# Optimization experiments

Measured on AMD Instinct MI355X. Metric: run time of the kernel, lower is better.

## Reference

```python
import jax, jax.numpy as jnp
import numpy as np

DROPOUT_RATE = 0.25
MASK_KEY = jax.random.key(42)

def _masks(key, shape, rate):
    keep = 1.0 - rate
    k1, k2, k3 = jax.random.split(key, 3)
    m = lambda k: jax.random.bernoulli(k, keep, shape).astype(jnp.float32) / keep
    return m(k1), m(k2), m(k3)  # out_mask, h_mask, c_mask

def _lstm_layer(x, W_ih, W_hh, b_ih, b_hh, layer_key, rate):
    # x: [B, T, D]; W_ih: [4H, D]; W_hh: [4H, H]
    B, T, _ = x.shape
    H = W_hh.shape[1]
    m_out, m_h, m_c = _masks(layer_key, (B, H), rate)  # variational: shared across time
    # Precompute input-to-gate projection for the whole sequence (one big GEMM).
    xg = jnp.einsum('btd,gd->tbg', x, W_ih) + (b_ih + b_hh)  # [T, B, 4H]

    def step(carry, xg_t):
        h, c = carry
        g = xg_t + h @ W_hh.T  # [B, 4H]
        i, f, gg, o = jnp.split(g, 4, axis=-1)
        i, f, o = jax.nn.sigmoid(i), jax.nn.sigmoid(f), jax.nn.sigmoid(o)
        c = f * c + i * jnp.tanh(gg)
        h = o * jnp.tanh(c)
        out = h * m_out
        return (h * m_h, c * m_c), out

    h0 = jnp.zeros((B, H), x.dtype)
    c0 = jnp.zeros((B, H), x.dtype)
    _, ys = jax.lax.scan(step, (h0, c0), xg)  # ys: [T, B, H]
    return jnp.transpose(ys, (1, 0, 2))  # [B, T, H]

def setup_inputs() -> dict:
    key = jax.random.key(0)
    ks = jax.random.split(key, 9)
    B, T, D, H = 64, 512, 256, 256
    s_ih = 1.0 / np.sqrt(D)
    s_hh = 1.0 / np.sqrt(H)
    return {
        'x': jax.random.normal(ks[0], (B, T, D), jnp.float32),
        'W_ih0': jax.random.uniform(ks[1], (4 * H, D), jnp.float32, -s_ih, s_ih),
        'W_hh0': jax.random.uniform(ks[2], (4 * H, H), jnp.float32, -s_hh, s_hh),
        'b_ih0': jax.random.uniform(ks[3], (4 * H,), jnp.float32, -s_hh, s_hh),
        'b_hh0': jax.random.uniform(ks[4], (4 * H,), jnp.float32, -s_hh, s_hh),
        'W_ih1': jax.random.uniform(ks[5], (4 * H, H), jnp.float32, -s_hh, s_hh),
        'W_hh1': jax.random.uniform(ks[6], (4 * H, H), jnp.float32, -s_hh, s_hh),
        'b_ih1': jax.random.uniform(ks[7], (4 * H,), jnp.float32, -s_hh, s_hh),
        'b_hh1': jax.random.uniform(ks[8], (4 * H,), jnp.float32, -s_hh, s_hh),
    }

def reference(x, W_ih0, W_hh0, b_ih0, b_hh0, W_ih1, W_hh1, b_ih1, b_hh1):
    k0, k1 = jax.random.split(MASK_KEY, 2)
    x = _lstm_layer(x, W_ih0, W_hh0, b_ih0, b_hh0, k0, DROPOUT_RATE)
    x = _lstm_layer(x, W_ih1, W_hh1, b_ih1, b_hh1, k1, DROPOUT_RATE)
    return x
```

## Files before the change

### kernel.cpp

```cpp
#include <hip/hip_runtime.h>

typedef unsigned int u32;
typedef unsigned short u16;

typedef short short8 __attribute__((ext_vector_type(8)));
typedef float f32x4 __attribute__((ext_vector_type(4)));


__device__ __forceinline__ float fast_exp2(float x) {
#if __has_builtin(__builtin_amdgcn_exp2f)
  return __builtin_amdgcn_exp2f(x);
#else
  return exp2f(x);
#endif
}
__device__ __forceinline__ float fast_rcp(float x) {
#if __has_builtin(__builtin_amdgcn_rcpf)
  return __builtin_amdgcn_rcpf(x);
#else
  return 1.0f / x;
#endif
}
__device__ __forceinline__ float sigmf_(float x) {
  return fast_rcp(1.0f + fast_exp2(-1.44269504088896f * x));
}
__device__ __forceinline__ float tanhf_(float x) {
  float e = fast_exp2(2.88539008177793f * x);
  return 1.0f - 2.0f * fast_rcp(e + 1.0f);
}
__device__ __forceinline__ u16 f2bf(float x) {
  u32 u = __float_as_uint(x);
  u32 r = (u + 0x7fffu + ((u >> 16) & 1u)) >> 16;
  return (u16)r;
}

#if __has_builtin(__builtin_amdgcn_fdot2_f32_bf16)
typedef __bf16 bf16x2_t __attribute__((ext_vector_type(2)));
__device__ __forceinline__ float dot2bf(u32 w, u32 h, float acc) {
  return __builtin_amdgcn_fdot2_f32_bf16(__builtin_bit_cast(bf16x2_t, w),
                                         __builtin_bit_cast(bf16x2_t, h), acc, false);
}
#else
__device__ __forceinline__ float dot2bf(u32 w, u32 h, float acc) {
  float wl = __uint_as_float(w << 16);
  float wh = __uint_as_float(w & 0xffff0000u);
  float hl = __uint_as_float(h << 16);
  float hh = __uint_as_float(h & 0xffff0000u);
  return fmaf(wh, hh, fmaf(wl, hl, acc));
}
#endif


__device__ __forceinline__ void tf_round(u32& x0, u32& x1, int r) {
  x0 += x1;
  x1 = (x1 << r) | (x1 >> (32 - r));
  x1 ^= x0;
}
__device__ void threefry(u32 k0, u32 k1, u32 c0, u32 c1, u32& o0, u32& o1) {
  u32 k2 = k0 ^ k1 ^ 0x1BD11BDAu;
  u32 x0 = c0 + k0, x1 = c1 + k1;
  tf_round(x0, x1, 13); tf_round(x0, x1, 15); tf_round(x0, x1, 26); tf_round(x0, x1, 6);
  x0 += k1; x1 += k2 + 1u;
  tf_round(x0, x1, 17); tf_round(x0, x1, 29); tf_round(x0, x1, 16); tf_round(x0, x1, 24);
  x0 += k2; x1 += k0 + 2u;
  tf_round(x0, x1, 13); tf_round(x0, x1, 15); tf_round(x0, x1, 26); tf_round(x0, x1, 6);
  x0 += k0; x1 += k1 + 3u;
  tf_round(x0, x1, 17); tf_round(x0, x1, 29); tf_round(x0, x1, 16); tf_round(x0, x1, 24);
  x0 += k1; x1 += k2 + 4u;
  tf_round(x0, x1, 13); tf_round(x0, x1, 15); tf_round(x0, x1, 26); tf_round(x0, x1, 6);
  x0 += k2; x1 += k0 + 5u;
  o0 = x0; o1 = x1;
}

#define JAX_PARTITIONABLE 1

__global__ void masks_kernel(float* __restrict__ masks) {
  int gid = blockIdx.x * 256 + threadIdx.x;
  if (gid >= 2 * 3 * 16384) return;
  int l = gid / 49152;
  int rem = gid - l * 49152;
  int typ = rem / 16384;
  int i = rem - typ * 16384;
  u32 bits;
#if JAX_PARTITIONABLE
  u32 lk0, lk1, mk0, mk1, y0, y1;
  threefry(0u, 42u, 0u, (u32)l, lk0, lk1);
  threefry(lk0, lk1, 0u, (u32)typ, mk0, mk1);
  threefry(mk0, mk1, 0u, (u32)i, y0, y1);
  bits = y0 ^ y1;
#else
  u32 a0, a1, b0, b1;
  threefry(0u, 42u, 0u, 2u, a0, a1);
  threefry(0u, 42u, 1u, 3u, b0, b1);
  u32 lk0 = (l == 0) ? a0 : a1;
  u32 lk1 = (l == 0) ? b0 : b1;
  u32 e00, e01, e10, e11, e20, e21;
  threefry(lk0, lk1, 0u, 3u, e00, e01);
  threefry(lk0, lk1, 1u, 4u, e10, e11);
  threefry(lk0, lk1, 2u, 5u, e20, e21);
  u32 mk0 = (typ == 0) ? e00 : (typ == 1) ? e20 : e11;
  u32 mk1 = (typ == 0) ? e10 : (typ == 1) ? e01 : e21;
  u32 p = (i < 8192) ? (u32)i : (u32)(i - 8192);
  u32 y0, y1;
  threefry(mk0, mk1, p, p + 8192u, y0, y1);
  bits = (i < 8192) ? y0 : y1;
#endif
  float u = __uint_as_float((bits >> 9) | 0x3f800000u) - 1.0f;
  masks[gid] = (u < 0.75f) ? (1.0f / 0.75f) : 0.0f;
}


__global__ void conv_bf16(const float* __restrict__ src, u16* __restrict__ dst, int n) {
  int gid = blockIdx.x * 256 + threadIdx.x;
  if (gid < n) dst[gid] = f2bf(src[gid]);
}

__global__ void pack_whh(const float* __restrict__ W, u32* __restrict__ Wp, u32* __restrict__ Ws) {
  int gid = blockIdx.x * 256 + threadIdx.x;
  int p = gid >> 10;
  int row = gid & 1023;
  u32 lo = f2bf(W[row * 256 + 2 * p]);
  u32 hi = f2bf(W[row * 256 + 2 * p + 1]);
  u32 v = lo | (hi << 16);
  Wp[p * 1024 + row] = v;
  if (p >= 112) Ws[row * 16 + (p - 112)] = v;
}

__global__ void add_bias(const float* __restrict__ a, const float* __restrict__ b,
                         float* __restrict__ o, int n) {
  int gid = blockIdx.x * 256 + threadIdx.x;
  if (gid < n) o[gid] = a[gid] + b[gid];
}

__global__ __launch_bounds__(256) void gemm_xg(const u16* __restrict__ A,
                                               const u16* __restrict__ Bw,
                                               float* __restrict__ xg) {
  __shared__ uint4 Als[2048];
  __shared__ uint4 Bls[2048];
  int tid = threadIdx.x;
  int m0 = blockIdx.x * 64;
  int n0 = blockIdx.y * 64;
  {
    int row = tid >> 2, kseg = tid & 3;
    const uint4* Ag = (const uint4*)(A + (size_t)(m0 + row) * 256);
    const uint4* Bg = (const uint4*)(Bw + (size_t)(n0 + row) * 256);
#pragma unroll
    for (int uu = 0; uu < 8; ++uu) {
      int kb = kseg * 8 + uu;
      Als[kb * 64 + row] = Ag[kb];
      Bls[kb * 64 + row] = Bg[kb];
    }
  }
  __syncthreads();
  int w = tid >> 6, l = tid & 63;
  int wm = (w >> 1) * 32, wn = (w & 1) * 32;
  int lm = l & 15, q = l >> 4;
  f32x4 acc00 = {0.f, 0.f, 0.f, 0.f}, acc01 = acc00, acc10 = acc00, acc11 = acc00;
#pragma unroll
  for (int ks = 0; ks < 8; ++ks) {
    int kb = ks * 4 + q;
    short8 a0 = __builtin_bit_cast(short8, Als[kb * 64 + wm + lm]);
    short8 a1 = __builtin_bit_cast(short8, Als[kb * 64 + wm + 16 + lm]);
    short8 b0 = __builtin_bit_cast(short8, Bls[kb * 64 + wn + lm]);
    short8 b1 = __builtin_bit_cast(short8, Bls[kb * 64 + wn + 16 + lm]);
    acc00 = __builtin_amdgcn_mfma_f32_16x16x32_bf16(a0, b0, acc00, 0, 0, 0);
    acc01 = __builtin_amdgcn_mfma_f32_16x16x32_bf16(a0, b1, acc01, 0, 0, 0);
    acc10 = __builtin_amdgcn_mfma_f32_16x16x32_bf16(a1, b0, acc10, 0, 0, 0);
    acc11 = __builtin_amdgcn_mfma_f32_16x16x32_bf16(a1, b1, acc11, 0, 0, 0);
  }
#pragma unroll
  for (int fm = 0; fm < 2; ++fm)
#pragma unroll
    for (int fn = 0; fn < 2; ++fn) {
      f32x4 acc = (fm == 0) ? ((fn == 0) ? acc00 : acc01) : ((fn == 0) ? acc10 : acc11);
#pragma unroll
      for (int r = 0; r < 4; ++r) {
        int m = m0 + wm + fm * 16 + q * 4 + r;
        int n = n0 + wn + fn * 16 + lm;
        int bb = m >> 9, tt = m & 511;
        xg[(size_t)tt * 65536 + (size_t)bb * 1024 + n] = acc[r];
      }
    }
}

#define REG_P 98
#define LDS_P 14

__global__ __launch_bounds__(512) void lstm_rec(
    const u32* __restrict__ Wp,
    const uint4* __restrict__ Ws,
    const float* __restrict__ xg,
    const float* __restrict__ bias,
    const float* __restrict__ masks,
    float* __restrict__ outF,
    u16* __restrict__ outB)
{
  __shared__ u32 Wl[LDS_P * 1024];
  __shared__ float gates[1024];
  __shared__ alignas(16) u16 hbf[256];

  const int tid = threadIdx.x;
  const int b = blockIdx.x;
  const int r0 = tid, r1 = tid + 512;

  u32 wreg[2 * REG_P];
#pragma unroll
  for (int p = 0; p < REG_P; ++p) wreg[p] = Wp[p * 1024 + r0];
#pragma unroll
  for (int p = 0; p < REG_P; ++p) wreg[REG_P + p] = Wp[p * 1024 + r1];

#pragma unroll
  for (int s = 0; s < LDS_P; ++s) {
    Wl[s * 1024 + r0] = Wp[(REG_P + s) * 1024 + r0];
    Wl[s * 1024 + r1] = Wp[(REG_P + s) * 1024 + r1];
  }
  if (tid < 256) hbf[tid] = 0;

  const float bias0 = bias[r0];
  const float bias1 = bias[r1];
  float c = 0.f, m_out = 0.f, m_h = 0.f, m_c = 0.f;
  if (tid < 256) {
    m_out = masks[0 * 16384 + b * 256 + tid];
    m_h   = masks[1 * 16384 + b * 256 + tid];
    m_c   = masks[2 * 16384 + b * 256 + tid];
  }
  const uint4* Wsr0 = Ws + (size_t)r0 * 4;
  const uint4* Wsr1 = Ws + (size_t)r1 * 4;
  const float* xgb = xg + b * 1024;
  float* outFb = outF ? outF + (size_t)b * 512 * 256 : (float*)0;
  u16* outBb = outB ? outB + (size_t)b * 512 * 256 : (u16*)0;

  __syncthreads();

  for (int t = 0; t < 512; ++t) {
    float xg0 = xgb[(size_t)t * 65536 + r0];
    float xg1 = xgb[(size_t)t * 65536 + r1];
    float acc0 = bias0, acc1 = bias1;
    const uint4* h4 = (const uint4*)hbf;
#pragma unroll
    for (int s4 = 0; s4 < 4; ++s4) {
      uint4 v0 = Wsr0[s4];
      uint4 v1 = Wsr1[s4];
      uint4 hp = h4[28 + s4];
      acc0 = dot2bf(v0.x, hp.x, acc0); acc1 = dot2bf(v1.x, hp.x, acc1);
      acc0 = dot2bf(v0.y, hp.y, acc0); acc1 = dot2bf(v1.y, hp.y, acc1);
      acc0 = dot2bf(v0.z, hp.z, acc0); acc1 = dot2bf(v1.z, hp.z, acc1);
      acc0 = dot2bf(v0.w, hp.w, acc0); acc1 = dot2bf(v1.w, hp.w, acc1);
    }
#pragma unroll
    for (int qq = 0; qq < 28; ++qq) {
      uint4 hp = h4[qq];
      u32 hh[4] = {hp.x, hp.y, hp.z, hp.w};
#pragma unroll
      for (int e = 0; e < 4; ++e) {
        const int p = qq * 4 + e;
        u32 w0, w1;
        if (p < REG_P) {
          w0 = wreg[p];
          w1 = wreg[REG_P + p];
        } else {
          w0 = Wl[(p - REG_P) * 1024 + r0];
          w1 = Wl[(p - REG_P) * 1024 + r1];
        }
        acc0 = dot2bf(w0, hh[e], acc0);
        acc1 = dot2bf(w1, hh[e], acc1);
      }
    }
    acc0 += xg0;
    acc1 += xg1;
    gates[r0] = acc0;
    gates[r1] = acc1;
    __syncthreads();
    if (tid < 256) {
      float gi = gates[tid];
      float gf = gates[tid + 256];
      float gg = gates[tid + 512];
      float go = gates[tid + 768];
      float fi = sigmf_(gi), ff = sigmf_(gf), fo = sigmf_(go);
      float tg = tanhf_(gg);
      c = ff * c + fi * tg;
      float hn = fo * tanhf_(c);
      float ov = hn * m_out;
      if (outFb) outFb[t * 256 + tid] = ov;
      if (outBb) outBb[t * 256 + tid] = f2bf(ov);
      hbf[tid] = f2bf(hn * m_h);
      c *= m_c;
    }
    __syncthreads();
  }
}


extern "C" void kernel_launch(void* const* d_in, const int* in_sizes, int n_in,
                              void* d_out, int out_size, void* d_ws, size_t ws_size,
                              hipStream_t stream) {
  const float* x    = (const float*)d_in[0];
  const float* Wih0 = (const float*)d_in[1];
  const float* Whh0 = (const float*)d_in[2];
  const float* bih0 = (const float*)d_in[3];
  const float* bhh0 = (const float*)d_in[4];
  const float* Wih1 = (const float*)d_in[5];
  const float* Whh1 = (const float*)d_in[6];
  const float* bih1 = (const float*)d_in[7];
  const float* bhh1 = (const float*)d_in[8];
  float* out = (float*)d_out;

  char* w = (char*)d_ws;
  float* masks = (float*)(w + 0);
  float* biasb = (float*)(w + 393216);
  u32* Wp0     = (u32*)(w + 401408);
  u32* Wp1     = (u32*)(w + 925696);
  u32* Ws0     = (u32*)(w + 1449984);
  u32* Ws1     = (u32*)(w + 1515520);
  u16* Wih0b   = (u16*)(w + 1581056);
  u16* Wih1b   = (u16*)(w + 2105344);
  u16* xb      = (u16*)(w + 2629632);
  u16* o1b     = (u16*)(w + 19406848);
  float* xg    = (float*)(w + 36184064);

  hipLaunchKernelGGL(masks_kernel, dim3(384), dim3(256), 0, stream, masks);
  hipLaunchKernelGGL(conv_bf16, dim3(32768), dim3(256), 0, stream, x, xb, 8388608);
  hipLaunchKernelGGL(conv_bf16, dim3(1024), dim3(256), 0, stream, Wih0, Wih0b, 262144);
  hipLaunchKernelGGL(conv_bf16, dim3(1024), dim3(256), 0, stream, Wih1, Wih1b, 262144);
  hipLaunchKernelGGL(pack_whh, dim3(512), dim3(256), 0, stream, Whh0, Wp0, Ws0);
  hipLaunchKernelGGL(pack_whh, dim3(512), dim3(256), 0, stream, Whh1, Wp1, Ws1);
  hipLaunchKernelGGL(add_bias, dim3(4), dim3(256), 0, stream, bih0, bhh0, biasb, 1024);
  hipLaunchKernelGGL(add_bias, dim3(4), dim3(256), 0, stream, bih1, bhh1, biasb + 1024, 1024);

  hipLaunchKernelGGL(gemm_xg, dim3(512, 16), dim3(256), 0, stream, xb, Wih0b, xg);
  hipLaunchKernelGGL(lstm_rec, dim3(64), dim3(512), 0, stream, Wp0, (const uint4*)Ws0, xg,
                     biasb, masks, (float*)nullptr, o1b);
  hipLaunchKernelGGL(gemm_xg, dim3(512, 16), dim3(256), 0, stream, o1b, Wih1b, xg);
  hipLaunchKernelGGL(lstm_rec, dim3(64), dim3(512), 0, stream, Wp1, (const uint4*)Ws1, xg,
                     biasb + 1024, masks + 49152, out, (u16*)nullptr);
}
```

Before: 1.944 ms.

## Give each recurrent thread all four gates of one unit to drop gate LDS sync

The recurrent kernel now runs 256 threads per batch row instead of 512. Each thread computes the i, f, g and o gate rows for one hidden unit and holds 96 packed weight pairs per gate in registers (384 VGPRs). The remaining 32 pairs per gate are streamed from a uint4-transposed global layout with double-buffered prefetch. Since the gate nonlinearity happens in the same thread, the shared gates array and one barrier per timestep go away, and h is double-buffered in LDS. This halves the thread count and greatly raises register pressure (risk of spills) to cut per-step synchronisation and idle half-block work.

```diff
diff --git a/kernel.cpp b/kernel.cpp
--- a/kernel.cpp
+++ b/kernel.cpp
@@ -115,15 +115,19 @@
   if (gid < n) dst[gid] = f2bf(src[gid]);
 }
 
-__global__ void pack_whh(const float* __restrict__ W, u32* __restrict__ Wp, u32* __restrict__ Ws) {
+__global__ void pack_whh(const float* __restrict__ W, u32* __restrict__ Wp, u32* __restrict__ Wst) {
   int gid = blockIdx.x * 256 + threadIdx.x;
   int p = gid >> 10;
   int row = gid & 1023;
   u32 lo = f2bf(W[row * 256 + 2 * p]);
   u32 hi = f2bf(W[row * 256 + 2 * p + 1]);
   u32 v = lo | (hi << 16);
-  Wp[p * 1024 + row] = v;
-  if (p >= 112) Ws[row * 16 + (p - 112)] = v;
+  if (p < 96) {
+    Wp[p * 1024 + row] = v;
+  } else {
+    int q = (p - 96) >> 2, e = (p - 96) & 3;
+    Wst[(q * 1024 + row) * 4 + e] = v;
+  }
 }
 
 __global__ void add_bias(const float* __restrict__ a, const float* __restrict__ b,
@@ -183,49 +187,41 @@
     }
 }
 
-#define REG_P 98
-#define LDS_P 14
-
-__global__ __launch_bounds__(512) void lstm_rec(
+#define REG_P 96
+
+__global__ __launch_bounds__(256, 1) void lstm_rec(
     const u32* __restrict__ Wp,
-    const uint4* __restrict__ Ws,
+    const uint4* __restrict__ Wst,
     const float* __restrict__ xg,
     const float* __restrict__ bias,
     const float* __restrict__ masks,
     float* __restrict__ outF,
     u16* __restrict__ outB)
 {
-  __shared__ u32 Wl[LDS_P * 1024];
-  __shared__ float gates[1024];
-  __shared__ alignas(16) u16 hbf[256];
+  __shared__ alignas(16) u16 hbf[2][256];
 
   const int tid = threadIdx.x;
   const int b = blockIdx.x;
-  const int r0 = tid, r1 = tid + 512;
-
-  u32 wreg[2 * REG_P];
-#pragma unroll
-  for (int p = 0; p < REG_P; ++p) wreg[p] = Wp[p * 1024 + r0];
-#pragma unroll
-  for (int p = 0; p < REG_P; ++p) wreg[REG_P + p] = Wp[p * 1024 + r1];
-
-#pragma unroll
-  for (int s = 0; s < LDS_P; ++s) {
-    Wl[s * 1024 + r0] = Wp[(REG_P + s) * 1024 + r0];
-    Wl[s * 1024 + r1] = Wp[(REG_P + s) * 1024 + r1];
-  }
-  if (tid < 256) hbf[tid] = 0;
-
-  const float bias0 = bias[r0];
-  const float bias1 = bias[r1];
-  float c = 0.f, m_out = 0.f, m_h = 0.f, m_c = 0.f;
-  if (tid < 256) {
-    m_out = masks[0 * 16384 + b * 256 + tid];
-    m_h   = masks[1 * 16384 + b * 256 + tid];
-    m_c   = masks[2 * 16384 + b * 256 + tid];
-  }
-  const uint4* Wsr0 = Ws + (size_t)r0 * 4;
-  const uint4* Wsr1 = Ws + (size_t)r1 * 4;
+
+  u32 wreg[4][REG_P];
+#pragma unroll
+  for (int g = 0; g < 4; ++g) {
+    const int row = tid + 256 * g;
+#pragma unroll
+    for (int p = 0; p < REG_P; ++p) wreg[g][p] = Wp[p * 1024 + row];
+  }
+
+  hbf[0][tid] = 0;
+
+  float biasv[4];
+#pragma unroll
+  for (int g = 0; g < 4; ++g) biasv[g] = bias[tid + 256 * g];
+
+  const float m_out = masks[0 * 16384 + b * 256 + tid];
+  const float m_h   = masks[1 * 16384 + b * 256 + tid];
+  const float m_c   = masks[2 * 16384 + b * 256 + tid];
+  float c = 0.f;
+
   const float* xgb = xg + b * 1024;
   float* outFb = outF ? outF + (size_t)b * 512 * 256 : (float*)0;
   u16* outBb = outB ? outB + (size_t)b * 512 * 256 : (u16*)0;
@@ -233,59 +229,63 @@
   __syncthreads();
 
   for (int t = 0; t < 512; ++t) {
-    float xg0 = xgb[(size_t)t * 65536 + r0];
-    float xg1 = xgb[(size_t)t * 65536 + r1];
-    float acc0 = bias0, acc1 = bias1;
-    const uint4* h4 = (const uint4*)hbf;
-#pragma unroll
-    for (int s4 = 0; s4 < 4; ++s4) {
-      uint4 v0 = Wsr0[s4];
-      uint4 v1 = Wsr1[s4];
-      uint4 hp = h4[28 + s4];
-      acc0 = dot2bf(v0.x, hp.x, acc0); acc1 = dot2bf(v1.x, hp.x, acc1);
-      acc0 = dot2bf(v0.y, hp.y, acc0); acc1 = dot2bf(v1.y, hp.y, acc1);
-      acc0 = dot2bf(v0.z, hp.z, acc0); acc1 = dot2bf(v1.z, hp.z, acc1);
-      acc0 = dot2bf(v0.w, hp.w, acc0); acc1 = dot2bf(v1.w, hp.w, acc1);
-    }
-#pragma unroll
-    for (int qq = 0; qq < 28; ++qq) {
-      uint4 hp = h4[qq];
-      u32 hh[4] = {hp.x, hp.y, hp.z, hp.w};
-#pragma unroll
-      for (int e = 0; e < 4; ++e) {
-        const int p = qq * 4 + e;
-        u32 w0, w1;
-        if (p < REG_P) {
-          w0 = wreg[p];
-          w1 = wreg[REG_P + p];
-        } else {
-          w0 = Wl[(p - REG_P) * 1024 + r0];
-          w1 = Wl[(p - REG_P) * 1024 + r1];
-        }
-        acc0 = dot2bf(w0, hh[e], acc0);
-        acc1 = dot2bf(w1, hh[e], acc1);
+    float xgv[4];
+#pragma unroll
+    for (int g = 0; g < 4; ++g) xgv[g] = xgb[(size_t)t * 65536 + tid + 256 * g];
+
+    const uint4* h4 = (const uint4*)hbf[t & 1];
+
+    float acc[4];
+#pragma unroll
+    for (int g = 0; g < 4; ++g) acc[g] = biasv[g];
+
+    uint4 tva[4], tvb[4];
+#pragma unroll
+    for (int g = 0; g < 4; ++g) tva[g] = Wst[0 * 1024 + tid + 256 * g];
+
+#pragma unroll
+    for (int q = 0; q < 24; ++q) {
+      uint4 hp = h4[q];
+#pragma unroll
+      for (int g = 0; g < 4; ++g) {
+        acc[g] = dot2bf(wreg[g][4 * q + 0], hp.x, acc[g]);
+        acc[g] = dot2bf(wreg[g][4 * q + 1], hp.y, acc[g]);
+        acc[g] = dot2bf(wreg[g][4 * q + 2], hp.z, acc[g]);
+        acc[g] = dot2bf(wreg[g][4 * q + 3], hp.w, acc[g]);
       }
     }
-    acc0 += xg0;
-    acc1 += xg1;
-    gates[r0] = acc0;
-    gates[r1] = acc1;
-    __syncthreads();
-    if (tid < 256) {
-      float gi = gates[tid];
-      float gf = gates[tid + 256];
-      float gg = gates[tid + 512];
-      float go = gates[tid + 768];
-      float fi = sigmf_(gi), ff = sigmf_(gf), fo = sigmf_(go);
-      float tg = tanhf_(gg);
-      c = ff * c + fi * tg;
-      float hn = fo * tanhf_(c);
-      float ov = hn * m_out;
-      if (outFb) outFb[t * 256 + tid] = ov;
-      if (outBb) outBb[t * 256 + tid] = f2bf(ov);
-      hbf[tid] = f2bf(hn * m_h);
-      c *= m_c;
+
+#pragma unroll
+    for (int q = 0; q < 8; ++q) {
+      uint4* curv = (q & 1) ? tvb : tva;
+      uint4* nxtv = (q & 1) ? tva : tvb;
+      if (q < 7) {
+#pragma unroll
+        for (int g = 0; g < 4; ++g) nxtv[g] = Wst[(q + 1) * 1024 + tid + 256 * g];
+      }
+      uint4 hp = h4[24 + q];
+#pragma unroll
+      for (int g = 0; g < 4; ++g) {
+        acc[g] = dot2bf(curv[g].x, hp.x, acc[g]);
+        acc[g] = dot2bf(curv[g].y, hp.y, acc[g]);
+        acc[g] = dot2bf(curv[g].z, hp.z, acc[g]);
+        acc[g] = dot2bf(curv[g].w, hp.w, acc[g]);
+      }
     }
+
+    float gi = acc[0] + xgv[0];
+    float gf = acc[1] + xgv[1];
+    float gg = acc[2] + xgv[2];
+    float go = acc[3] + xgv[3];
+    float fi = sigmf_(gi), ff = sigmf_(gf), fo = sigmf_(go);
+    float tg = tanhf_(gg);
+    c = ff * c + fi * tg;
+    float hn = fo * tanhf_(c);
+    float ov = hn * m_out;
+    if (outFb) outFb[t * 256 + tid] = ov;
+    if (outBb) outBb[t * 256 + tid] = f2bf(ov);
+    hbf[(t + 1) & 1][tid] = f2bf(hn * m_h);
+    c *= m_c;
     __syncthreads();
   }
 }
@@ -309,28 +309,28 @@
   float* masks = (float*)(w + 0);
   float* biasb = (float*)(w + 393216);
   u32* Wp0     = (u32*)(w + 401408);
-  u32* Wp1     = (u32*)(w + 925696);
-  u32* Ws0     = (u32*)(w + 1449984);
-  u32* Ws1     = (u32*)(w + 1515520);
-  u16* Wih0b   = (u16*)(w + 1581056);
-  u16* Wih1b   = (u16*)(w + 2105344);
-  u16* xb      = (u16*)(w + 2629632);
-  u16* o1b     = (u16*)(w + 19406848);
-  float* xg    = (float*)(w + 36184064);
+  u32* Wp1     = (u32*)(w + 794624);
+  u32* Wst0    = (u32*)(w + 1187840);
+  u32* Wst1    = (u32*)(w + 1318912);
+  u16* Wih0b   = (u16*)(w + 1449984);
+  u16* Wih1b   = (u16*)(w + 1974272);
+  u16* xb      = (u16*)(w + 2498560);
+  u16* o1b     = (u16*)(w + 19275776);
+  float* xg    = (float*)(w + 36052992);
 
   hipLaunchKernelGGL(masks_kernel, dim3(384), dim3(256), 0, stream, masks);
   hipLaunchKernelGGL(conv_bf16, dim3(32768), dim3(256), 0, stream, x, xb, 8388608);
   hipLaunchKernelGGL(conv_bf16, dim3(1024), dim3(256), 0, stream, Wih0, Wih0b, 262144);
   hipLaunchKernelGGL(conv_bf16, dim3(1024), dim3(256), 0, stream, Wih1, Wih1b, 262144);
-  hipLaunchKernelGGL(pack_whh, dim3(512), dim3(256), 0, stream, Whh0, Wp0, Ws0);
-  hipLaunchKernelGGL(pack_whh, dim3(512), dim3(256), 0, stream, Whh1, Wp1, Ws1);
+  hipLaunchKernelGGL(pack_whh, dim3(512), dim3(256), 0, stream, Whh0, Wp0, Wst0);
+  hipLaunchKernelGGL(pack_whh, dim3(512), dim3(256), 0, stream, Whh1, Wp1, Wst1);
   hipLaunchKernelGGL(add_bias, dim3(4), dim3(256), 0, stream, bih0, bhh0, biasb, 1024);
   hipLaunchKernelGGL(add_bias, dim3(4), dim3(256), 0, stream, bih1, bhh1, biasb + 1024, 1024);
 
   hipLaunchKernelGGL(gemm_xg, dim3(512, 16), dim3(256), 0, stream, xb, Wih0b, xg);
-  hipLaunchKernelGGL(lstm_rec, dim3(64), dim3(512), 0, stream, Wp0, (const uint4*)Ws0, xg,
+  hipLaunchKernelGGL(lstm_rec, dim3(64), dim3(256), 0, stream, Wp0, (const uint4*)Wst0, xg,
                      biasb, masks, (float*)nullptr, o1b);
   hipLaunchKernelGGL(gemm_xg, dim3(512, 16), dim3(256), 0, stream, o1b, Wih1b, xg);
-  hipLaunchKernelGGL(lstm_rec, dim3(64), dim3(512), 0, stream, Wp1, (const uint4*)Ws1, xg,
+  hipLaunchKernelGGL(lstm_rec, dim3(64), dim3(256), 0, stream, Wp1, (const uint4*)Wst1, xg,
                      biasb + 1024, masks + 49152, out, (u16*)nullptr);
 }
```

Result: slower. 5.716 ms (+194.0%).

## Use 1024-thread recurrent blocks with one gate row per thread in registers

Applied to the files above, without the earlier changes.

The recurrent kernel now launches 1024 threads per batch element, so each thread owns one gate row. Its 128 packed bf16 weight pairs are held entirely in registers as 32 uint4, which removes the LDS weight tier and the separate global 'Ws' tail read on every step. The W_hh packing is changed to a q-major uint4 layout to match, and the next step's xg value is prefetched one iteration ahead. In exchange, each block now has twice as many waves syncing at every step, and only 256 of the 1024 threads do the elementwise gate work.

```diff
diff --git a/kernel.cpp b/kernel.cpp
--- a/kernel.cpp
+++ b/kernel.cpp
@@ -115,15 +115,15 @@
   if (gid < n) dst[gid] = f2bf(src[gid]);
 }
 
-__global__ void pack_whh(const float* __restrict__ W, u32* __restrict__ Wp, u32* __restrict__ Ws) {
+__global__ void pack_whh(const float* __restrict__ W, u32* __restrict__ Wq) {
   int gid = blockIdx.x * 256 + threadIdx.x;
   int p = gid >> 10;
   int row = gid & 1023;
   u32 lo = f2bf(W[row * 256 + 2 * p]);
   u32 hi = f2bf(W[row * 256 + 2 * p + 1]);
   u32 v = lo | (hi << 16);
-  Wp[p * 1024 + row] = v;
-  if (p >= 112) Ws[row * 16 + (p - 112)] = v;
+  int q = p >> 2, e = p & 3;
+  Wq[(q * 1024 + row) * 4 + e] = v;
 }
 
 __global__ void add_bias(const float* __restrict__ a, const float* __restrict__ b,
@@ -183,94 +183,59 @@
     }
 }
 
-#define REG_P 98
-#define LDS_P 14
-
-__global__ __launch_bounds__(512) void lstm_rec(
-    const u32* __restrict__ Wp,
-    const uint4* __restrict__ Ws,
+__global__ __launch_bounds__(1024, 4) void lstm_rec(
+    const uint4* __restrict__ Wq,
     const float* __restrict__ xg,
     const float* __restrict__ bias,
     const float* __restrict__ masks,
     float* __restrict__ outF,
     u16* __restrict__ outB)
 {
-  __shared__ u32 Wl[LDS_P * 1024];
   __shared__ float gates[1024];
   __shared__ alignas(16) u16 hbf[256];
 
   const int tid = threadIdx.x;
   const int b = blockIdx.x;
-  const int r0 = tid, r1 = tid + 512;
-
-  u32 wreg[2 * REG_P];
-#pragma unroll
-  for (int p = 0; p < REG_P; ++p) wreg[p] = Wp[p * 1024 + r0];
-#pragma unroll
-  for (int p = 0; p < REG_P; ++p) wreg[REG_P + p] = Wp[p * 1024 + r1];
-
-#pragma unroll
-  for (int s = 0; s < LDS_P; ++s) {
-    Wl[s * 1024 + r0] = Wp[(REG_P + s) * 1024 + r0];
-    Wl[s * 1024 + r1] = Wp[(REG_P + s) * 1024 + r1];
-  }
+
+  uint4 w[32];
+#pragma unroll
+  for (int q = 0; q < 32; ++q) w[q] = Wq[q * 1024 + tid];
+
   if (tid < 256) hbf[tid] = 0;
 
-  const float bias0 = bias[r0];
-  const float bias1 = bias[r1];
+  const float biasv = bias[tid];
   float c = 0.f, m_out = 0.f, m_h = 0.f, m_c = 0.f;
   if (tid < 256) {
     m_out = masks[0 * 16384 + b * 256 + tid];
     m_h   = masks[1 * 16384 + b * 256 + tid];
     m_c   = masks[2 * 16384 + b * 256 + tid];
   }
-  const uint4* Wsr0 = Ws + (size_t)r0 * 4;
-  const uint4* Wsr1 = Ws + (size_t)r1 * 4;
-  const float* xgb = xg + b * 1024;
-  float* outFb = outF ? outF + (size_t)b * 512 * 256 : (float*)0;
-  u16* outBb = outB ? outB + (size_t)b * 512 * 256 : (u16*)0;
-
+
+  const float* xgp = xg + b * 1024 + tid;
+  float* outFp = outF ? outF + (size_t)b * 512 * 256 + tid : (float*)0;
+  u16* outBp = outB ? outB + (size_t)b * 512 * 256 + tid : (u16*)0;
+
+  float xg_next = xgp[0];
   __syncthreads();
 
+#pragma unroll 1
   for (int t = 0; t < 512; ++t) {
-    float xg0 = xgb[(size_t)t * 65536 + r0];
-    float xg1 = xgb[(size_t)t * 65536 + r1];
-    float acc0 = bias0, acc1 = bias1;
+    float xgv = xg_next;
+    if (t < 511) xg_next = xgp[(size_t)(t + 1) * 65536];
+
     const uint4* h4 = (const uint4*)hbf;
-#pragma unroll
-    for (int s4 = 0; s4 < 4; ++s4) {
-      uint4 v0 = Wsr0[s4];
-      uint4 v1 = Wsr1[s4];
-      uint4 hp = h4[28 + s4];
-      acc0 = dot2bf(v0.x, hp.x, acc0); acc1 = dot2bf(v1.x, hp.x, acc1);
-      acc0 = dot2bf(v0.y, hp.y, acc0); acc1 = dot2bf(v1.y, hp.y, acc1);
-      acc0 = dot2bf(v0.z, hp.z, acc0); acc1 = dot2bf(v1.z, hp.z, acc1);
-      acc0 = dot2bf(v0.w, hp.w, acc0); acc1 = dot2bf(v1.w, hp.w, acc1);
-    }
-#pragma unroll
-    for (int qq = 0; qq < 28; ++qq) {
-      uint4 hp = h4[qq];
-      u32 hh[4] = {hp.x, hp.y, hp.z, hp.w};
-#pragma unroll
-      for (int e = 0; e < 4; ++e) {
-        const int p = qq * 4 + e;
-        u32 w0, w1;
-        if (p < REG_P) {
-          w0 = wreg[p];
-          w1 = wreg[REG_P + p];
-        } else {
-          w0 = Wl[(p - REG_P) * 1024 + r0];
-          w1 = Wl[(p - REG_P) * 1024 + r1];
-        }
-        acc0 = dot2bf(w0, hh[e], acc0);
-        acc1 = dot2bf(w1, hh[e], acc1);
-      }
-    }
-    acc0 += xg0;
-    acc1 += xg1;
-    gates[r0] = acc0;
-    gates[r1] = acc1;
+    float acc = biasv;
+#pragma unroll
+    for (int q = 0; q < 32; ++q) {
+      uint4 hp = h4[q];
+      acc = dot2bf(w[q].x, hp.x, acc);
+      acc = dot2bf(w[q].y, hp.y, acc);
+      acc = dot2bf(w[q].z, hp.z, acc);
+      acc = dot2bf(w[q].w, hp.w, acc);
+    }
+    gates[tid] = acc + xgv;
     __syncthreads();
+
     if (tid < 256) {
       float gi = gates[tid];
       float gf = gates[tid + 256];
@@ -281,8 +246,8 @@
       c = ff * c + fi * tg;
       float hn = fo * tanhf_(c);
       float ov = hn * m_out;
-      if (outFb) outFb[t * 256 + tid] = ov;
-      if (outBb) outBb[t * 256 + tid] = f2bf(ov);
+      if (outFp) outFp[t * 256] = ov;
+      if (outBp) outBp[t * 256] = f2bf(ov);
       hbf[tid] = f2bf(hn * m_h);
       c *= m_c;
     }
@@ -308,29 +273,27 @@
   char* w = (char*)d_ws;
   float* masks = (float*)(w + 0);
   float* biasb = (float*)(w + 393216);
-  u32* Wp0     = (u32*)(w + 401408);
-  u32* Wp1     = (u32*)(w + 925696);
-  u32* Ws0     = (u32*)(w + 1449984);
-  u32* Ws1     = (u32*)(w + 1515520);
-  u16* Wih0b   = (u16*)(w + 1581056);
-  u16* Wih1b   = (u16*)(w + 2105344);
-  u16* xb      = (u16*)(w + 2629632);
-  u16* o1b     = (u16*)(w + 19406848);
-  float* xg    = (float*)(w + 36184064);
+  u32* Wq0     = (u32*)(w + 401408);
+  u32* Wq1     = (u32*)(w + 925696);
+  u16* Wih0b   = (u16*)(w + 1449984);
+  u16* Wih1b   = (u16*)(w + 1974272);
+  u16* xb      = (u16*)(w + 2498560);
+  u16* o1b     = (u16*)(w + 19275776);
+  float* xg    = (float*)(w + 36052992);
 
   hipLaunchKernelGGL(masks_kernel, dim3(384), dim3(256), 0, stream, masks);
   hipLaunchKernelGGL(conv_bf16, dim3(32768), dim3(256), 0, stream, x, xb, 8388608);
   hipLaunchKernelGGL(conv_bf16, dim3(1024), dim3(256), 0, stream, Wih0, Wih0b, 262144);
   hipLaunchKernelGGL(conv_bf16, dim3(1024), dim3(256), 0, stream, Wih1, Wih1b, 262144);
-  hipLaunchKernelGGL(pack_whh, dim3(512), dim3(256), 0, stream, Whh0, Wp0, Ws0);
-  hipLaunchKernelGGL(pack_whh, dim3(512), dim3(256), 0, stream, Whh1, Wp1, Ws1);
+  hipLaunchKernelGGL(pack_whh, dim3(512), dim3(256), 0, stream, Whh0, Wq0);
+  hipLaunchKernelGGL(pack_whh, dim3(512), dim3(256), 0, stream, Whh1, Wq1);
   hipLaunchKernelGGL(add_bias, dim3(4), dim3(256), 0, stream, bih0, bhh0, biasb, 1024);
   hipLaunchKernelGGL(add_bias, dim3(4), dim3(256), 0, stream, bih1, bhh1, biasb + 1024, 1024);
 
   hipLaunchKernelGGL(gemm_xg, dim3(512, 16), dim3(256), 0, stream, xb, Wih0b, xg);
-  hipLaunchKernelGGL(lstm_rec, dim3(64), dim3(512), 0, stream, Wp0, (const uint4*)Ws0, xg,
+  hipLaunchKernelGGL(lstm_rec, dim3(64), dim3(1024), 0, stream, (const uint4*)Wq0, xg,
                      biasb, masks, (float*)nullptr, o1b);
   hipLaunchKernelGGL(gemm_xg, dim3(512, 16), dim3(256), 0, stream, o1b, Wih1b, xg);
-  hipLaunchKernelGGL(lstm_rec, dim3(64), dim3(512), 0, stream, Wp1, (const uint4*)Ws1, xg,
+  hipLaunchKernelGGL(lstm_rec, dim3(64), dim3(1024), 0, stream, (const uint4*)Wq1, xg,
                      biasb + 1024, masks + 49152, out, (u16*)nullptr);
 }
```

New measurement: 4.301 ms. 121% more time.
